# Kernel optimization log

Hardware: AMD Instinct MI355X
Metric: run time of the kernel (lower is better)

## Reference

```python
import jax, jax.numpy as jnp
import numpy as np

L, P = 8, 512
HID = 128
N_COARSE, N_FINE = 64, 128
LVIS_NEAR, LVIS_FAR = 1e-3, 0.5
S = 100.0  # 1 / fixed_s_recp


def _mlp_sdf(x, w0, b0, w1, b1, w2, b2, w3, b3):
    # x: [..., 3] -> sdf [...]
    h = jax.nn.relu(x @ w0 + b0)
    h = jax.nn.relu(h @ w1 + b1)
    h = jax.nn.relu(h @ w2 + b2)
    return (h @ w3 + b3)[..., 0]


def _sdf_to_w(sdf, s):
    # faithful to sdf_to_w: cdf -> alpha -> visibility weights via cumprod
    cdf = jax.nn.sigmoid(sdf * s)
    alpha = jnp.clip((cdf[..., :-1] - cdf[..., 1:]) / (cdf[..., :-1] + 1e-10), 0.0, None)
    ones = jnp.ones(alpha.shape[:-1] + (1,), alpha.dtype)
    shifted = jnp.concatenate([ones, 1.0 - alpha + 1e-10], axis=-1)
    return alpha * jnp.cumprod(shifted, axis=-1)[..., :-1]


def _sample_pdf(bins, weights, u):
    # standard NeRF importance sampling; bins [...,M+1], weights [...,M], u [...,N]
    weights = weights + 1e-5
    pdf = weights / jnp.sum(weights, axis=-1, keepdims=True)
    cdf = jnp.cumsum(pdf, axis=-1)
    cdf = jnp.concatenate([jnp.zeros_like(cdf[..., :1]), cdf], axis=-1)  # [...,M+1]
    # searchsorted (right) via broadcast compare: [...,N,M+1]
    inds = jnp.sum((u[..., None] >= cdf[..., None, :]).astype(jnp.int32), axis=-1)
    below = jnp.clip(inds - 1, 0, cdf.shape[-1] - 1)
    above = jnp.clip(inds, 0, cdf.shape[-1] - 1)
    cdf_b = jnp.take_along_axis(cdf, below, axis=-1)
    cdf_a = jnp.take_along_axis(cdf, above, axis=-1)
    bins_b = jnp.take_along_axis(bins, below, axis=-1)
    bins_a = jnp.take_along_axis(bins, above, axis=-1)
    denom = cdf_a - cdf_b
    denom = jnp.where(denom < 1e-5, jnp.ones_like(denom), denom)
    t = (u - cdf_b) / denom
    return bins_b + t * (bins_a - bins_b)


def setup_inputs() -> dict:
    key = jax.random.key(0)
    ks = jax.random.split(key, 8)

    def lin(k, fi, fo):
        return jax.random.normal(k, (fi, fo), jnp.float32) / jnp.sqrt(jnp.float32(fi))

    return {
        "pts": jax.random.normal(ks[0], (1, P, 3), jnp.float32) * 0.5,
        "light_posi": jax.random.normal(ks[1], (L, 3), jnp.float32) * 2.0,
        "u": jax.random.uniform(ks[2], (L, P, N_FINE), jnp.float32),
        "w0": lin(ks[3], 3, HID), "b0": jnp.zeros((HID,), jnp.float32),
        "w1": lin(ks[4], HID, HID), "b1": jnp.zeros((HID,), jnp.float32),
        "w2": lin(ks[5], HID, HID), "b2": jnp.zeros((HID,), jnp.float32),
        "w3": lin(ks[6], HID, 1), "b3": jnp.zeros((1,), jnp.float32),
    }


def reference(pts, light_posi, u, w0, b0, w1, b1, w2, b2, w3, b3):
    sdf = lambda x: _mlp_sdf(x, w0, b0, w1, b1, w2, b2, w3, b3)
    # pts: [1,P,3]; light_posi: [L,3]
    pts2l = light_posi[:, None, :] - pts  # [L,P,3]
    pts2l = pts2l / jnp.linalg.norm(pts2l, axis=-1, keepdims=True)
    t = jnp.linspace(0.0, 1.0 - 1.0 / N_COARSE, N_COARSE, dtype=jnp.float32)
    d_coarse = LVIS_NEAR * (1.0 - t) + LVIS_FAR * t  # [N_COARSE]
    d_coarse = jnp.broadcast_to(d_coarse, (pts2l.shape[0], pts.shape[1], N_COARSE))
    # coarse sample points: [L,P,Nc,3]
    pts_coarse = pts[:, :, None, :] + d_coarse[..., None] * pts2l[:, :, None, :]
    w_coarse = _sdf_to_w(sdf(pts_coarse), S)  # [L,P,Nc-1]
    d_fine = _sample_pdf(d_coarse, w_coarse, u)  # [L,P,Nf]
    d_all = jnp.sort(jnp.concatenate([d_coarse, d_fine], axis=-1), axis=-1)  # [L,P,Nc+Nf]
    pts_all = pts[:, :, None, :] + d_all[..., None] * pts2l[:, :, None, :]
    w_all = _sdf_to_w(sdf(pts_all), S)
    occu = jnp.sum(w_all, axis=-1)  # [L,P]
    return 1.0 - occu
```

## Files before the change

kernel.cpp:

```cpp
#include <hip/hip_runtime.h>
#include <math.h>

#define NL 8
#define NP 512
#define NC 64
#define NF 128
#define NALL 192
#define NRAY (NL * NP)
#define HID 128

typedef _Float16 half8 __attribute__((ext_vector_type(8)));
typedef _Float16 half4v __attribute__((ext_vector_type(4)));
typedef float floatx16 __attribute__((ext_vector_type(16)));
typedef unsigned long long ull;

#define MFMA(a, b, c) __builtin_amdgcn_mfma_f32_32x32x16_f16((a), (b), (c), 0, 0, 0)


__device__ __forceinline__ float dcoarse_at(int i) {
    float t = (float)i * 0.015625f;
    return 1e-3f * (1.0f - t) + 0.5f * t;
}

__device__ __forceinline__ floatx16 fzero16() {
    floatx16 z;
#pragma unroll
    for (int i = 0; i < 16; ++i) z[i] = 0.f;
    return z;
}
__device__ __forceinline__ half8 hzero8() {
    half8 z;
#pragma unroll
    for (int i = 0; i < 8; ++i) z[i] = (_Float16)0.f;
    return z;
}

__global__ void prep_kernel(const float* __restrict__ w1, const float* __restrict__ w2,
                            _Float16* __restrict__ Wsp) {
    int f = blockIdx.x * 256 + threadIdx.x;
    int layer = blockIdx.y;
    const float* w = layer ? w2 : w1;
    int i = f & 7, l31 = (f >> 3) & 31, lhi = (f >> 8) & 1, ks = (f >> 9) & 7, jb = f >> 12;
    int j = jb * 32 + l31;
    int k = ks * 16 + lhi * 8 + i;
    float v = w[k * 128 + j];
    _Float16 hi = (_Float16)v;
    Wsp[(layer * 2 + 0) * 16384 + f] = hi;
    Wsp[(layer * 2 + 1) * 16384 + f] = (_Float16)(v - (float)hi);
}

template<int MODE, int FASTW>
__global__ __launch_bounds__(512, 4) void mlp_kernel(
    const float* __restrict__ pts, const float* __restrict__ lights,
    const float* __restrict__ d_fine,
    const float* __restrict__ w0, const float* __restrict__ b0,
    const float* __restrict__ w1, const float* __restrict__ b1,
    const float* __restrict__ w2, const float* __restrict__ b2,
    const float* __restrict__ w3, const float* __restrict__ b3,
    const _Float16* __restrict__ Wsp,
    float* __restrict__ sdf_out)
{
    __shared__ __align__(16) _Float16 H[2 * 128 * 128];
    __shared__ _Float16 Xs[6 * 128];
    __shared__ float P2[4 * 128];

    const int tid = threadIdx.x;
    const int lane = tid & 63;
    const int wv = tid >> 6;
    const int jq = wv & 3, mh = wv >> 2;
    const int l31 = lane & 31, lhi = lane >> 5;
    const int base = blockIdx.x * 128;

    if (tid < 128) {
        int pt = base + tid;
        int ray; float d;
        if (MODE == 0) { ray = pt >> 6; d = dcoarse_at(pt & 63); }
        else           { ray = pt >> 7; d = d_fine[pt]; }
        int l = ray >> 9, p = ray & (NP - 1);
        float px = pts[p * 3 + 0], py = pts[p * 3 + 1], pz = pts[p * 3 + 2];
        float dx = lights[l * 3 + 0] - px, dy = lights[l * 3 + 1] - py, dz = lights[l * 3 + 2] - pz;
        float n = sqrtf(dx * dx + dy * dy + dz * dz);
        dx /= n; dy /= n; dz /= n;
        float xc[3] = { px + d * dx, py + d * dy, pz + d * dz };
#pragma unroll
        for (int c = 0; c < 3; ++c) {
            _Float16 h = (_Float16)xc[c];
            Xs[c * 128 + tid] = h;
            Xs[(3 + c) * 128 + tid] = (_Float16)(xc[c] - (float)h);
        }
    }

    const int m0 = mh * 64;
    const int mrow0 = m0 + l31;
    char* Hb = (char*)H;

    int rdoff[8];
#pragma unroll
    for (int ks = 0; ks < 8; ++ks) {
        int k0 = ks * 16 + lhi * 8;
        rdoff[ks] = (mrow0 * 128 + ((((k0 >> 3) ^ (mrow0 & 15)) << 3) | (k0 & 7))) * 2;
    }

    auto store_tile = [&](const floatx16& a, int mt, const float* __restrict__ bias) {
        int mrow = mrow0 + mt * 32;
#pragma unroll
        for (int g = 0; g < 4; ++g) {
            int jg = jq * 32 + 8 * g + 4 * lhi;
            half4v hq, lq;
#pragma unroll
            for (int q = 0; q < 4; ++q) {
                float v = fmaxf(a[g * 4 + q] + bias[jg + q], 0.f);
                _Float16 hi = (_Float16)v;
                hq[q] = hi;
                lq[q] = (_Float16)(v - (float)hi);
            }
            int ad = (mrow * 128 + ((((jg >> 3) ^ (mrow & 15)) << 3) | (jg & 7))) * 2;
            *(half4v*)(Hb + ad) = hq;
            *(half4v*)(Hb + ad + 32768) = lq;
        }
    };

    floatx16 acc[2];

    const int aoff = jq * 4096 + lhi * 256 + l31 * 8 + 2048;
    const _Float16* pA0h = Wsp + 0 * 16384 + aoff;
    const _Float16* pA0l = Wsp + 1 * 16384 + aoff;
    const _Float16* pA1h = Wsp + 2 * 16384 + aoff;
    const _Float16* pA1l = Wsp + 3 * 16384 + aoff;

    auto ldA_slow = [&](int L, int ks, half8& ah, half8& al) {
        const float* w = L ? w2 : w1;
        int j = jq * 32 + l31, k0 = ks * 16 + lhi * 8;
#pragma unroll
        for (int i = 0; i < 8; ++i) {
            float v = w[(k0 + i) * 128 + j];
            _Float16 hi = (_Float16)v;
            ah[i] = hi;
            al[i] = (_Float16)(v - (float)hi);
        }
    };

    half8 Ah[8], Al[8];
    auto preload4 = [&](int L, const _Float16* ph, const _Float16* pl) {
        if (FASTW) {
#pragma unroll
            for (int ks = 0; ks < 4; ++ks) {
                Ah[ks] = *(const half8*)(ph + ks * 512 - 2048);
                Al[ks] = *(const half8*)(pl + ks * 512 - 2048);
            }
        } else {
#pragma unroll
            for (int ks = 0; ks < 4; ++ks) ldA_slow(L, ks, Ah[ks], Al[ks]);
        }
    };

    auto gemm = [&](int L, const _Float16* ph, const _Float16* pl) {
        acc[0] = fzero16(); acc[1] = fzero16();
#pragma unroll
        for (int ks = 0; ks < 8; ++ks) {
            if (ks < 4) {
                if (FASTW) {
                    Ah[ks + 4] = *(const half8*)(ph + (ks + 4) * 512 - 2048);
                    Al[ks + 4] = *(const half8*)(pl + (ks + 4) * 512 - 2048);
                } else {
                    ldA_slow(L, ks + 4, Ah[ks + 4], Al[ks + 4]);
                }
            }
            char* ba = Hb + rdoff[ks];
            half8 bh0 = *(const half8*)(ba);
            half8 bh1 = *(const half8*)(ba + 8192);
            half8 bl0 = *(const half8*)(ba + 32768);
            half8 bl1 = *(const half8*)(ba + 40960);
            acc[0] = MFMA(Al[ks], bh0, acc[0]); acc[1] = MFMA(Al[ks], bh1, acc[1]);
            acc[0] = MFMA(Ah[ks], bl0, acc[0]); acc[1] = MFMA(Ah[ks], bl1, acc[1]);
            acc[0] = MFMA(Ah[ks], bh0, acc[0]); acc[1] = MFMA(Ah[ks], bh1, acc[1]);
        }
    };

    __syncthreads();

    {
        half8 a1h = hzero8(), a1l = hzero8(), bh1[2], bl1[2];
        bh1[0] = hzero8(); bh1[1] = hzero8(); bl1[0] = hzero8(); bl1[1] = hzero8();
        if (lhi == 0) {
            int j = jq * 32 + l31;
#pragma unroll
            for (int c = 0; c < 3; ++c) {
                float v = w0[c * 128 + j];
                _Float16 hi = (_Float16)v;
                a1h[c] = hi;
                a1l[c] = (_Float16)(v - (float)hi);
            }
#pragma unroll
            for (int mt = 0; mt < 2; ++mt) {
                int m = m0 + mt * 32 + l31;
#pragma unroll
                for (int c = 0; c < 3; ++c) {
                    bh1[mt][c] = Xs[c * 128 + m];
                    bl1[mt][c] = Xs[(3 + c) * 128 + m];
                }
            }
        }
        acc[0] = fzero16(); acc[1] = fzero16();
        acc[0] = MFMA(a1l, bh1[0], acc[0]); acc[1] = MFMA(a1l, bh1[1], acc[1]);
        acc[0] = MFMA(a1h, bl1[0], acc[0]); acc[1] = MFMA(a1h, bl1[1], acc[1]);
        acc[0] = MFMA(a1h, bh1[0], acc[0]); acc[1] = MFMA(a1h, bh1[1], acc[1]);
        store_tile(acc[0], 0, b0);
        store_tile(acc[1], 1, b0);
    }

    preload4(0, pA0h, pA0l);
    __syncthreads();

    gemm(0, pA0h, pA0l);
    preload4(1, pA1h, pA1l);
    __syncthreads();
    store_tile(acc[0], 0, b1);
    store_tile(acc[1], 1, b1);
    __syncthreads();

    gemm(1, pA1h, pA1l);
#pragma unroll
    for (int mt = 0; mt < 2; ++mt) {
        float p = 0.f;
#pragma unroll
        for (int g = 0; g < 4; ++g) {
            int jg = jq * 32 + 8 * g + 4 * lhi;
#pragma unroll
            for (int q = 0; q < 4; ++q) {
                float v = fmaxf(acc[mt][g * 4 + q] + b2[jg + q], 0.f);
                p = fmaf(v, w3[jg + q], p);
            }
        }
        p += __shfl_xor(p, 32);
        if (lane < 32) P2[jq * 128 + m0 + mt * 32 + l31] = p;
    }
    __syncthreads();
    if (tid < 128)
        sdf_out[base + tid] = b3[0] + P2[tid] + P2[128 + tid] + P2[256 + tid] + P2[384 + tid];
}

__global__ __launch_bounds__(256) void sample_kernel(
    const float* __restrict__ sdf_c, const float* __restrict__ u,
    float* __restrict__ d_fine, unsigned char* __restrict__ perm8) {
    const int lane = threadIdx.x & 63, wv = threadIdx.x >> 6;
    const int ray = blockIdx.x * 4 + wv;

    float sv = sdf_c[ray * NC + lane];
    float c = 1.0f / (1.0f + expf(-100.0f * sv));
    float cn = __shfl_down(c, 1);
    bool valid = lane < 63;
    float a = valid ? fmaxf((c - cn) / (c + 1e-10f), 0.f) : 0.f;
    float sh = valid ? (1.f - a + 1e-10f) : 1.f;
    float ps = sh;
#pragma unroll
    for (int off = 1; off < 64; off <<= 1) { float o = __shfl_up(ps, off); if (lane >= off) ps *= o; }
    float T = __shfl_up(ps, 1);
    if (lane == 0) T = 1.f;
    float w = valid ? (a * T + 1e-5f) : 0.f;
    float wsum = w;
#pragma unroll
    for (int off = 1; off < 64; off <<= 1) wsum += __shfl_xor(wsum, off);
    float pdf = w / wsum;
    float cs = pdf;
#pragma unroll
    for (int off = 1; off < 64; off <<= 1) { float o = __shfl_up(cs, off); if (lane >= off) cs += o; }
    float cdfv = __shfl_up(cs, 1);
    if (lane == 0) cdfv = 0.f;

    float df[2];
#pragma unroll
    for (int t = 0; t < 2; ++t) {
        float uu = u[ray * NF + t * 64 + lane];
        int lo = 0;
#pragma unroll
        for (int b = 32; b >= 1; b >>= 1) {
            float cm = __shfl(cdfv, lo + b);
            if (uu >= cm) lo += b;
        }
        int above = min(lo + 1, NC - 1);
        float cb = __shfl(cdfv, lo), ca = __shfl(cdfv, above);
        float bb = dcoarse_at(lo), ba = dcoarse_at(above);
        float denom = ca - cb;
        if (denom < 1e-5f) denom = 1.f;
        float tt = (uu - cb) / denom;
        df[t] = bb + tt * (ba - bb);
        d_fine[ray * 128 + t * 64 + lane] = df[t];
    }

    ull v[4];
    v[0] = ((ull)__float_as_uint(dcoarse_at(lane)) << 32) | (unsigned)lane;
    v[1] = ((ull)__float_as_uint(df[0]) << 32) | (unsigned)(64 + lane);
    v[2] = ((ull)__float_as_uint(df[1]) << 32) | (unsigned)(128 + lane);
    v[3] = ((ull)0x7F800000u << 32) | 255u;
    for (int k = 2; k <= 256; k <<= 1) {
        for (int j = k >> 1; j > 0; j >>= 1) {
            if (j >= 64) {
                int tj = j >> 6;
#pragma unroll
                for (int t = 0; t < 4; ++t) {
                    if ((t & tj) == 0) {
                        int t2 = t ^ tj;
                        bool asc = (((t * 64) & k) == 0);
                        ull x = v[t], y = v[t2];
                        bool sw = asc ? (x > y) : (x < y);
                        if (sw) { v[t] = y; v[t2] = x; }
                    }
                }
            } else {
#pragma unroll
                for (int t = 0; t < 4; ++t) {
                    int i = t * 64 + lane;
                    ull other = __shfl_xor(v[t], j);
                    bool lower = (lane & j) == 0;
                    bool asc = ((i & k) == 0);
                    bool takeMin = (lower == asc);
                    ull mn = v[t] < other ? v[t] : other;
                    ull mx = v[t] < other ? other : v[t];
                    v[t] = takeMin ? mn : mx;
                }
            }
        }
    }
#pragma unroll
    for (int t = 0; t < 3; ++t)
        perm8[ray * NALL + t * 64 + lane] = (unsigned char)(v[t] & 0xFFu);
}

__global__ __launch_bounds__(256) void finish_kernel(
    const float* __restrict__ sdf_c, const float* __restrict__ sdf_f,
    const unsigned char* __restrict__ perm8, float* __restrict__ out) {
    int lane = threadIdx.x & 63, wv = threadIdx.x >> 6;
    int ray = blockIdx.x * 4 + wv;
    const unsigned char* P = perm8 + (size_t)ray * NALL;
    float c[4];
#pragma unroll
    for (int t = 0; t < 4; ++t) {
        int i = lane * 3 + t;
        if (i < NALL) {
            int idx = P[i];
            float s = (idx < 64) ? sdf_c[ray * NC + idx] : sdf_f[ray * 128 + (idx - 64)];
            c[t] = 1.0f / (1.0f + expf(-100.0f * s));
        } else c[t] = 0.f;
    }
    float a[3], s[3];
#pragma unroll
    for (int t = 0; t < 3; ++t) {
        int i = lane * 3 + t;
        if (i < NALL - 1) {
            a[t] = fmaxf((c[t] - c[t + 1]) / (c[t] + 1e-10f), 0.f);
            s[t] = 1.f - a[t] + 1e-10f;
        } else { a[t] = 0.f; s[t] = 1.f; }
    }
    float chunk = s[0] * s[1] * s[2];
    float ps = chunk;
#pragma unroll
    for (int off = 1; off < 64; off <<= 1) {
        float o = __shfl_up(ps, off);
        if (lane >= off) ps *= o;
    }
    float T = __shfl_up(ps, 1);
    if (lane == 0) T = 1.f;
    float occ = a[0] * T;
    T *= s[0]; occ = fmaf(a[1], T, occ);
    T *= s[1]; occ = fmaf(a[2], T, occ);
#pragma unroll
    for (int off = 1; off < 64; off <<= 1) occ += __shfl_xor(occ, off);
    if (lane == 0) out[ray] = 1.f - occ;
}

extern "C" void kernel_launch(void* const* d_in, const int* in_sizes, int n_in,
                              void* d_out, int out_size, void* d_ws, size_t ws_size,
                              hipStream_t stream) {
    const float* pts = (const float*)d_in[0];
    const float* lights = (const float*)d_in[1];
    const float* u = (const float*)d_in[2];
    const float* w0 = (const float*)d_in[3];
    const float* b0 = (const float*)d_in[4];
    const float* w1 = (const float*)d_in[5];
    const float* b1 = (const float*)d_in[6];
    const float* w2 = (const float*)d_in[7];
    const float* b2 = (const float*)d_in[8];
    const float* w3 = (const float*)d_in[9];
    const float* b3 = (const float*)d_in[10];
    float* out = (float*)d_out;

    char* wsb = (char*)d_ws;
    float* sdf_c = (float*)wsb;
    float* sdf_f = (float*)(wsb + (size_t)NRAY * NC * 4);
    float* d_fine = (float*)(wsb + (size_t)NRAY * (NC + 128) * 4);
    unsigned char* perm8 = (unsigned char*)(wsb + (size_t)NRAY * (NC + 256) * 4);
    _Float16* Wsp = (_Float16*)(wsb + (size_t)NRAY * (NC + 256) * 4 + (size_t)NRAY * NALL);
    const size_t need = (size_t)NRAY * (NC + 256) * 4 + (size_t)NRAY * NALL
                      + (size_t)4 * 16384 * sizeof(_Float16);
    const bool fast = ws_size >= need;

    if (fast) {
        prep_kernel<<<dim3(64, 2), 256, 0, stream>>>(w1, w2, Wsp);
        mlp_kernel<0, 1><<<(NRAY * NC) / 128, 512, 0, stream>>>(
            pts, lights, nullptr, w0, b0, w1, b1, w2, b2, w3, b3, Wsp, sdf_c);
        sample_kernel<<<NRAY / 4, 256, 0, stream>>>(sdf_c, u, d_fine, perm8);
        mlp_kernel<1, 1><<<(NRAY * 128) / 128, 512, 0, stream>>>(
            pts, lights, d_fine, w0, b0, w1, b1, w2, b2, w3, b3, Wsp, sdf_f);
    } else {
        mlp_kernel<0, 0><<<(NRAY * NC) / 128, 512, 0, stream>>>(
            pts, lights, nullptr, w0, b0, w1, b1, w2, b2, w3, b3, nullptr, sdf_c);
        sample_kernel<<<NRAY / 4, 256, 0, stream>>>(sdf_c, u, d_fine, perm8);
        mlp_kernel<1, 0><<<(NRAY * 128) / 128, 512, 0, stream>>>(
            pts, lights, d_fine, w0, b0, w1, b1, w2, b2, w3, b3, nullptr, sdf_f);
    }
    finish_kernel<<<NRAY / 4, 256, 0, stream>>>(sdf_c, sdf_f, perm8, out);
}
```

Before: 243.1 us.

## Halve MLP block to 4 waves, each computing 64x64 output tile

The MLP kernel now runs 256 threads (4 waves) per 128-point block instead of 512. Each wave computes two 32-column output tiles across two 32-row tiles, so every B fragment read from LDS feeds twice as many MFMAs. This halves LDS read traffic per MFMA. The register preloading of weight A fragments is replaced by per-k-step global loads. In exchange the kernel has fewer waves per block, a larger accumulator per wave that raises register pressure, and less latency hiding on the weight loads.

Result: no change. 244.3 us (+0.5%).

```diff
diff --git a/kernel.cpp b/kernel.cpp
--- a/kernel.cpp
+++ b/kernel.cpp
@@ -50,7 +50,7 @@
 }
 
 template<int MODE, int FASTW>
-__global__ __launch_bounds__(512, 4) void mlp_kernel(
+__global__ __launch_bounds__(256, 2) void mlp_kernel(
     const float* __restrict__ pts, const float* __restrict__ lights,
     const float* __restrict__ d_fine,
     const float* __restrict__ w0, const float* __restrict__ b0,
@@ -67,7 +67,7 @@
     const int tid = threadIdx.x;
     const int lane = tid & 63;
     const int wv = tid >> 6;
-    const int jq = wv & 3, mh = wv >> 2;
+    const int jh = wv & 1, mh = wv >> 1;
     const int l31 = lane & 31, lhi = lane >> 5;
     const int base = blockIdx.x * 128;
 
@@ -101,11 +101,11 @@
         rdoff[ks] = (mrow0 * 128 + ((((k0 >> 3) ^ (mrow0 & 15)) << 3) | (k0 & 7))) * 2;
     }
 
-    auto store_tile = [&](const floatx16& a, int mt, const float* __restrict__ bias) {
+    auto store_tile = [&](const floatx16& a, int jt, int mt, const float* __restrict__ bias) {
         int mrow = mrow0 + mt * 32;
 #pragma unroll
         for (int g = 0; g < 4; ++g) {
-            int jg = jq * 32 + 8 * g + 4 * lhi;
+            int jg = jh * 64 + jt * 32 + 8 * g + 4 * lhi;
             half4v hq, lq;
 #pragma unroll
             for (int q = 0; q < 4; ++q) {
@@ -120,17 +120,22 @@
         }
     };
 
-    floatx16 acc[2];
-
-    const int aoff = jq * 4096 + lhi * 256 + l31 * 8 + 2048;
-    const _Float16* pA0h = Wsp + 0 * 16384 + aoff;
-    const _Float16* pA0l = Wsp + 1 * 16384 + aoff;
-    const _Float16* pA1h = Wsp + 2 * 16384 + aoff;
-    const _Float16* pA1l = Wsp + 3 * 16384 + aoff;
-
-    auto ldA_slow = [&](int L, int ks, half8& ah, half8& al) {
+    floatx16 acc[2][2];
+
+    const int aoff0 = (jh * 2 + 0) * 4096 + lhi * 256 + l31 * 8 + 2048;
+    const int aoff1 = (jh * 2 + 1) * 4096 + lhi * 256 + l31 * 8 + 2048;
+    const _Float16* pA0h0 = Wsp + 0 * 16384 + aoff0;
+    const _Float16* pA0l0 = Wsp + 1 * 16384 + aoff0;
+    const _Float16* pA0h1 = Wsp + 0 * 16384 + aoff1;
+    const _Float16* pA0l1 = Wsp + 1 * 16384 + aoff1;
+    const _Float16* pA1h0 = Wsp + 2 * 16384 + aoff0;
+    const _Float16* pA1l0 = Wsp + 3 * 16384 + aoff0;
+    const _Float16* pA1h1 = Wsp + 2 * 16384 + aoff1;
+    const _Float16* pA1l1 = Wsp + 3 * 16384 + aoff1;
+
+    auto ldA_slow = [&](int L, int jt, int ks, half8& ah, half8& al) {
         const float* w = L ? w2 : w1;
-        int j = jq * 32 + l31, k0 = ks * 16 + lhi * 8;
+        int j = jh * 64 + jt * 32 + l31, k0 = ks * 16 + lhi * 8;
 #pragma unroll
         for (int i = 0; i < 8; ++i) {
             float v = w[(k0 + i) * 128 + j];
@@ -140,56 +145,53 @@
         }
     };
 
-    half8 Ah[8], Al[8];
-    auto preload4 = [&](int L, const _Float16* ph, const _Float16* pl) {
-        if (FASTW) {
-#pragma unroll
-            for (int ks = 0; ks < 4; ++ks) {
-                Ah[ks] = *(const half8*)(ph + ks * 512 - 2048);
-                Al[ks] = *(const half8*)(pl + ks * 512 - 2048);
-            }
-        } else {
-#pragma unroll
-            for (int ks = 0; ks < 4; ++ks) ldA_slow(L, ks, Ah[ks], Al[ks]);
-        }
-    };
-
-    auto gemm = [&](int L, const _Float16* ph, const _Float16* pl) {
-        acc[0] = fzero16(); acc[1] = fzero16();
+    auto gemm = [&](int L, const _Float16* ph0, const _Float16* pl0,
+                    const _Float16* ph1, const _Float16* pl1) {
+        acc[0][0] = fzero16(); acc[0][1] = fzero16();
+        acc[1][0] = fzero16(); acc[1][1] = fzero16();
 #pragma unroll
         for (int ks = 0; ks < 8; ++ks) {
-            if (ks < 4) {
-                if (FASTW) {
-                    Ah[ks + 4] = *(const half8*)(ph + (ks + 4) * 512 - 2048);
-                    Al[ks + 4] = *(const half8*)(pl + (ks + 4) * 512 - 2048);
-                } else {
-                    ldA_slow(L, ks + 4, Ah[ks + 4], Al[ks + 4]);
-                }
+            half8 a0h, a0l, a1h, a1l;
+            if (FASTW) {
+                a0h = *(const half8*)(ph0 + ks * 512 - 2048);
+                a0l = *(const half8*)(pl0 + ks * 512 - 2048);
+                a1h = *(const half8*)(ph1 + ks * 512 - 2048);
+                a1l = *(const half8*)(pl1 + ks * 512 - 2048);
+            } else {
+                ldA_slow(L, 0, ks, a0h, a0l);
+                ldA_slow(L, 1, ks, a1h, a1l);
             }
             char* ba = Hb + rdoff[ks];
             half8 bh0 = *(const half8*)(ba);
             half8 bh1 = *(const half8*)(ba + 8192);
             half8 bl0 = *(const half8*)(ba + 32768);
             half8 bl1 = *(const half8*)(ba + 40960);
-            acc[0] = MFMA(Al[ks], bh0, acc[0]); acc[1] = MFMA(Al[ks], bh1, acc[1]);
-            acc[0] = MFMA(Ah[ks], bl0, acc[0]); acc[1] = MFMA(Ah[ks], bl1, acc[1]);
-            acc[0] = MFMA(Ah[ks], bh0, acc[0]); acc[1] = MFMA(Ah[ks], bh1, acc[1]);
+            acc[0][0] = MFMA(a0l, bh0, acc[0][0]); acc[0][1] = MFMA(a0l, bh1, acc[0][1]);
+            acc[1][0] = MFMA(a1l, bh0, acc[1][0]); acc[1][1] = MFMA(a1l, bh1, acc[1][1]);
+            acc[0][0] = MFMA(a0h, bl0, acc[0][0]); acc[0][1] = MFMA(a0h, bl1, acc[0][1]);
+            acc[1][0] = MFMA(a1h, bl0, acc[1][0]); acc[1][1] = MFMA(a1h, bl1, acc[1][1]);
+            acc[0][0] = MFMA(a0h, bh0, acc[0][0]); acc[0][1] = MFMA(a0h, bh1, acc[0][1]);
+            acc[1][0] = MFMA(a1h, bh0, acc[1][0]); acc[1][1] = MFMA(a1h, bh1, acc[1][1]);
         }
     };
 
     __syncthreads();
 
     {
-        half8 a1h = hzero8(), a1l = hzero8(), bh1[2], bl1[2];
+        half8 a1h[2], a1l[2], bh1[2], bl1[2];
+        a1h[0] = hzero8(); a1h[1] = hzero8(); a1l[0] = hzero8(); a1l[1] = hzero8();
         bh1[0] = hzero8(); bh1[1] = hzero8(); bl1[0] = hzero8(); bl1[1] = hzero8();
         if (lhi == 0) {
-            int j = jq * 32 + l31;
-#pragma unroll
-            for (int c = 0; c < 3; ++c) {
-                float v = w0[c * 128 + j];
-                _Float16 hi = (_Float16)v;
-                a1h[c] = hi;
-                a1l[c] = (_Float16)(v - (float)hi);
+#pragma unroll
+            for (int jt = 0; jt < 2; ++jt) {
+                int j = jh * 64 + jt * 32 + l31;
+#pragma unroll
+                for (int c = 0; c < 3; ++c) {
+                    float v = w0[c * 128 + j];
+                    _Float16 hi = (_Float16)v;
+                    a1h[jt][c] = hi;
+                    a1l[jt][c] = (_Float16)(v - (float)hi);
+                }
             }
 #pragma unroll
             for (int mt = 0; mt < 2; ++mt) {
@@ -201,39 +203,47 @@
                 }
             }
         }
-        acc[0] = fzero16(); acc[1] = fzero16();
-        acc[0] = MFMA(a1l, bh1[0], acc[0]); acc[1] = MFMA(a1l, bh1[1], acc[1]);
-        acc[0] = MFMA(a1h, bl1[0], acc[0]); acc[1] = MFMA(a1h, bl1[1], acc[1]);
-        acc[0] = MFMA(a1h, bh1[0], acc[0]); acc[1] = MFMA(a1h, bh1[1], acc[1]);
-        store_tile(acc[0], 0, b0);
-        store_tile(acc[1], 1, b0);
-    }
-
-    preload4(0, pA0h, pA0l);
+        acc[0][0] = fzero16(); acc[0][1] = fzero16();
+        acc[1][0] = fzero16(); acc[1][1] = fzero16();
+        acc[0][0] = MFMA(a1l[0], bh1[0], acc[0][0]); acc[0][1] = MFMA(a1l[0], bh1[1], acc[0][1]);
+        acc[1][0] = MFMA(a1l[1], bh1[0], acc[1][0]); acc[1][1] = MFMA(a1l[1], bh1[1], acc[1][1]);
+        acc[0][0] = MFMA(a1h[0], bl1[0], acc[0][0]); acc[0][1] = MFMA(a1h[0], bl1[1], acc[0][1]);
+        acc[1][0] = MFMA(a1h[1], bl1[0], acc[1][0]); acc[1][1] = MFMA(a1h[1], bl1[1], acc[1][1]);
+        acc[0][0] = MFMA(a1h[0], bh1[0], acc[0][0]); acc[0][1] = MFMA(a1h[0], bh1[1], acc[0][1]);
+        acc[1][0] = MFMA(a1h[1], bh1[0], acc[1][0]); acc[1][1] = MFMA(a1h[1], bh1[1], acc[1][1]);
+        store_tile(acc[0][0], 0, 0, b0);
+        store_tile(acc[0][1], 0, 1, b0);
+        store_tile(acc[1][0], 1, 0, b0);
+        store_tile(acc[1][1], 1, 1, b0);
+    }
     __syncthreads();
 
-    gemm(0, pA0h, pA0l);
-    preload4(1, pA1h, pA1l);
+    gemm(0, pA0h0, pA0l0, pA0h1, pA0l1);
     __syncthreads();
-    store_tile(acc[0], 0, b1);
-    store_tile(acc[1], 1, b1);
+    store_tile(acc[0][0], 0, 0, b1);
+    store_tile(acc[0][1], 0, 1, b1);
+    store_tile(acc[1][0], 1, 0, b1);
+    store_tile(acc[1][1], 1, 1, b1);
     __syncthreads();
 
-    gemm(1, pA1h, pA1l);
-#pragma unroll
-    for (int mt = 0; mt < 2; ++mt) {
-        float p = 0.f;
-#pragma unroll
-        for (int g = 0; g < 4; ++g) {
-            int jg = jq * 32 + 8 * g + 4 * lhi;
-#pragma unroll
-            for (int q = 0; q < 4; ++q) {
-                float v = fmaxf(acc[mt][g * 4 + q] + b2[jg + q], 0.f);
-                p = fmaf(v, w3[jg + q], p);
-            }
-        }
-        p += __shfl_xor(p, 32);
-        if (lane < 32) P2[jq * 128 + m0 + mt * 32 + l31] = p;
+    gemm(1, pA1h0, pA1l0, pA1h1, pA1l1);
+#pragma unroll
+    for (int jt = 0; jt < 2; ++jt) {
+#pragma unroll
+        for (int mt = 0; mt < 2; ++mt) {
+            float p = 0.f;
+#pragma unroll
+            for (int g = 0; g < 4; ++g) {
+                int jg = jh * 64 + jt * 32 + 8 * g + 4 * lhi;
+#pragma unroll
+                for (int q = 0; q < 4; ++q) {
+                    float v = fmaxf(acc[jt][mt][g * 4 + q] + b2[jg + q], 0.f);
+                    p = fmaf(v, w3[jg + q], p);
+                }
+            }
+            p += __shfl_xor(p, 32);
+            if (lane < 32) P2[(jh * 2 + jt) * 128 + m0 + mt * 32 + l31] = p;
+        }
     }
     __syncthreads();
     if (tid < 128)
@@ -397,16 +407,16 @@
 
     if (fast) {
         prep_kernel<<<dim3(64, 2), 256, 0, stream>>>(w1, w2, Wsp);
-        mlp_kernel<0, 1><<<(NRAY * NC) / 128, 512, 0, stream>>>(
+        mlp_kernel<0, 1><<<(NRAY * NC) / 128, 256, 0, stream>>>(
             pts, lights, nullptr, w0, b0, w1, b1, w2, b2, w3, b3, Wsp, sdf_c);
         sample_kernel<<<NRAY / 4, 256, 0, stream>>>(sdf_c, u, d_fine, perm8);
-        mlp_kernel<1, 1><<<(NRAY * 128) / 128, 512, 0, stream>>>(
+        mlp_kernel<1, 1><<<(NRAY * 128) / 128, 256, 0, stream>>>(
             pts, lights, d_fine, w0, b0, w1, b1, w2, b2, w3, b3, Wsp, sdf_f);
     } else {
-        mlp_kernel<0, 0><<<(NRAY * NC) / 128, 512, 0, stream>>>(
+        mlp_kernel<0, 0><<<(NRAY * NC) / 128, 256, 0, stream>>>(
             pts, lights, nullptr, w0, b0, w1, b1, w2, b2, w3, b3, nullptr, sdf_c);
         sample_kernel<<<NRAY / 4, 256, 0, stream>>>(sdf_c, u, d_fine, perm8);
-        mlp_kernel<1, 0><<<(NRAY * 128) / 128, 512, 0, stream>>>(
+        mlp_kernel<1, 0><<<(NRAY * 128) / 128, 256, 0, stream>>>(
             pts, lights, d_fine, w0, b0, w1, b1, w2, b2, w3, b3, nullptr, sdf_f);
     }
     finish_kernel<<<NRAY / 4, 256, 0, stream>>>(sdf_c, sdf_f, perm8, out);
```

## Fuse importance sampling and final compositing into the MLP kernels

Applied to the files above, without the earlier changes.

The sampling step (CDF, inverse-CDF search, bitonic sort into a permutation) now runs as a tail of the coarse MLP kernel, and the final visibility compositing runs as a tail of the fine MLP kernel, using the fine SDF values still held in shared memory. This removes two kernel launches and the global round trip for the fine SDF buffer. The A-weight register preload across GEMMs is also dropped in favour of per-step loads, which cuts register pressure but exposes load latency. Only a few waves do the tail work while the rest of each 512-thread block sits idle.

Result: slower. 262.8 us (+8.1%).

```diff
diff --git a/kernel.cpp b/kernel.cpp
--- a/kernel.cpp
+++ b/kernel.cpp
@@ -52,13 +52,14 @@
 template<int MODE, int FASTW>
 __global__ __launch_bounds__(512, 4) void mlp_kernel(
     const float* __restrict__ pts, const float* __restrict__ lights,
-    const float* __restrict__ d_fine,
     const float* __restrict__ w0, const float* __restrict__ b0,
     const float* __restrict__ w1, const float* __restrict__ b1,
     const float* __restrict__ w2, const float* __restrict__ b2,
     const float* __restrict__ w3, const float* __restrict__ b3,
     const _Float16* __restrict__ Wsp,
-    float* __restrict__ sdf_out)
+    float* __restrict__ sdf_c, float* __restrict__ d_fine,
+    const float* __restrict__ u, unsigned char* __restrict__ perm8,
+    float* __restrict__ out)
 {
     __shared__ __align__(16) _Float16 H[2 * 128 * 128];
     __shared__ _Float16 Xs[6 * 128];
@@ -140,40 +141,25 @@
         }
     };
 
-    half8 Ah[8], Al[8];
-    auto preload4 = [&](int L, const _Float16* ph, const _Float16* pl) {
-        if (FASTW) {
-#pragma unroll
-            for (int ks = 0; ks < 4; ++ks) {
-                Ah[ks] = *(const half8*)(ph + ks * 512 - 2048);
-                Al[ks] = *(const half8*)(pl + ks * 512 - 2048);
-            }
-        } else {
-#pragma unroll
-            for (int ks = 0; ks < 4; ++ks) ldA_slow(L, ks, Ah[ks], Al[ks]);
-        }
-    };
-
     auto gemm = [&](int L, const _Float16* ph, const _Float16* pl) {
         acc[0] = fzero16(); acc[1] = fzero16();
 #pragma unroll
         for (int ks = 0; ks < 8; ++ks) {
-            if (ks < 4) {
-                if (FASTW) {
-                    Ah[ks + 4] = *(const half8*)(ph + (ks + 4) * 512 - 2048);
-                    Al[ks + 4] = *(const half8*)(pl + (ks + 4) * 512 - 2048);
-                } else {
-                    ldA_slow(L, ks + 4, Ah[ks + 4], Al[ks + 4]);
-                }
+            half8 ah, al;
+            if (FASTW) {
+                ah = *(const half8*)(ph + ks * 512 - 2048);
+                al = *(const half8*)(pl + ks * 512 - 2048);
+            } else {
+                ldA_slow(L, ks, ah, al);
             }
             char* ba = Hb + rdoff[ks];
             half8 bh0 = *(const half8*)(ba);
             half8 bh1 = *(const half8*)(ba + 8192);
             half8 bl0 = *(const half8*)(ba + 32768);
             half8 bl1 = *(const half8*)(ba + 40960);
-            acc[0] = MFMA(Al[ks], bh0, acc[0]); acc[1] = MFMA(Al[ks], bh1, acc[1]);
-            acc[0] = MFMA(Ah[ks], bl0, acc[0]); acc[1] = MFMA(Ah[ks], bl1, acc[1]);
-            acc[0] = MFMA(Ah[ks], bh0, acc[0]); acc[1] = MFMA(Ah[ks], bh1, acc[1]);
+            acc[0] = MFMA(al, bh0, acc[0]); acc[1] = MFMA(al, bh1, acc[1]);
+            acc[0] = MFMA(ah, bl0, acc[0]); acc[1] = MFMA(ah, bl1, acc[1]);
+            acc[0] = MFMA(ah, bh0, acc[0]); acc[1] = MFMA(ah, bh1, acc[1]);
         }
     };
 
@@ -208,12 +194,9 @@
         store_tile(acc[0], 0, b0);
         store_tile(acc[1], 1, b0);
     }
-
-    preload4(0, pA0h, pA0l);
     __syncthreads();
 
     gemm(0, pA0h, pA0l);
-    preload4(1, pA1h, pA1l);
     __syncthreads();
     store_tile(acc[0], 0, b1);
     store_tile(acc[1], 1, b1);
@@ -236,137 +219,136 @@
         if (lane < 32) P2[jq * 128 + m0 + mt * 32 + l31] = p;
     }
     __syncthreads();
-    if (tid < 128)
-        sdf_out[base + tid] = b3[0] + P2[tid] + P2[128 + tid] + P2[256 + tid] + P2[384 + tid];
-}
-
-__global__ __launch_bounds__(256) void sample_kernel(
-    const float* __restrict__ sdf_c, const float* __restrict__ u,
-    float* __restrict__ d_fine, unsigned char* __restrict__ perm8) {
-    const int lane = threadIdx.x & 63, wv = threadIdx.x >> 6;
-    const int ray = blockIdx.x * 4 + wv;
-
-    float sv = sdf_c[ray * NC + lane];
-    float c = 1.0f / (1.0f + expf(-100.0f * sv));
-    float cn = __shfl_down(c, 1);
-    bool valid = lane < 63;
-    float a = valid ? fmaxf((c - cn) / (c + 1e-10f), 0.f) : 0.f;
-    float sh = valid ? (1.f - a + 1e-10f) : 1.f;
-    float ps = sh;
-#pragma unroll
-    for (int off = 1; off < 64; off <<= 1) { float o = __shfl_up(ps, off); if (lane >= off) ps *= o; }
-    float T = __shfl_up(ps, 1);
-    if (lane == 0) T = 1.f;
-    float w = valid ? (a * T + 1e-5f) : 0.f;
-    float wsum = w;
-#pragma unroll
-    for (int off = 1; off < 64; off <<= 1) wsum += __shfl_xor(wsum, off);
-    float pdf = w / wsum;
-    float cs = pdf;
-#pragma unroll
-    for (int off = 1; off < 64; off <<= 1) { float o = __shfl_up(cs, off); if (lane >= off) cs += o; }
-    float cdfv = __shfl_up(cs, 1);
-    if (lane == 0) cdfv = 0.f;
-
-    float df[2];
-#pragma unroll
-    for (int t = 0; t < 2; ++t) {
-        float uu = u[ray * NF + t * 64 + lane];
-        int lo = 0;
-#pragma unroll
-        for (int b = 32; b >= 1; b >>= 1) {
-            float cm = __shfl(cdfv, lo + b);
-            if (uu >= cm) lo += b;
-        }
-        int above = min(lo + 1, NC - 1);
-        float cb = __shfl(cdfv, lo), ca = __shfl(cdfv, above);
-        float bb = dcoarse_at(lo), ba = dcoarse_at(above);
-        float denom = ca - cb;
-        if (denom < 1e-5f) denom = 1.f;
-        float tt = (uu - cb) / denom;
-        df[t] = bb + tt * (ba - bb);
-        d_fine[ray * 128 + t * 64 + lane] = df[t];
-    }
-
-    ull v[4];
-    v[0] = ((ull)__float_as_uint(dcoarse_at(lane)) << 32) | (unsigned)lane;
-    v[1] = ((ull)__float_as_uint(df[0]) << 32) | (unsigned)(64 + lane);
-    v[2] = ((ull)__float_as_uint(df[1]) << 32) | (unsigned)(128 + lane);
-    v[3] = ((ull)0x7F800000u << 32) | 255u;
-    for (int k = 2; k <= 256; k <<= 1) {
-        for (int j = k >> 1; j > 0; j >>= 1) {
-            if (j >= 64) {
-                int tj = j >> 6;
-#pragma unroll
-                for (int t = 0; t < 4; ++t) {
-                    if ((t & tj) == 0) {
-                        int t2 = t ^ tj;
-                        bool asc = (((t * 64) & k) == 0);
-                        ull x = v[t], y = v[t2];
-                        bool sw = asc ? (x > y) : (x < y);
-                        if (sw) { v[t] = y; v[t2] = x; }
+    if (tid < 128) {
+        float s = b3[0] + P2[tid] + P2[128 + tid] + P2[256 + tid] + P2[384 + tid];
+        if (MODE == 0) sdf_c[base + tid] = s;
+        P2[tid] = s;
+    }
+    __syncthreads();
+
+    if (MODE == 0) {
+        if (wv < 2) {
+            const int ray = blockIdx.x * 2 + wv;
+            float sv = P2[wv * 64 + lane];
+            float c = 1.0f / (1.0f + expf(-100.0f * sv));
+            float cn = __shfl_down(c, 1);
+            bool valid = lane < 63;
+            float a = valid ? fmaxf((c - cn) / (c + 1e-10f), 0.f) : 0.f;
+            float sh = valid ? (1.f - a + 1e-10f) : 1.f;
+            float ps = sh;
+#pragma unroll
+            for (int off = 1; off < 64; off <<= 1) { float o = __shfl_up(ps, off); if (lane >= off) ps *= o; }
+            float T = __shfl_up(ps, 1);
+            if (lane == 0) T = 1.f;
+            float w = valid ? (a * T + 1e-5f) : 0.f;
+            float wsum = w;
+#pragma unroll
+            for (int off = 1; off < 64; off <<= 1) wsum += __shfl_xor(wsum, off);
+            float pdf = w / wsum;
+            float cs = pdf;
+#pragma unroll
+            for (int off = 1; off < 64; off <<= 1) { float o = __shfl_up(cs, off); if (lane >= off) cs += o; }
+            float cdfv = __shfl_up(cs, 1);
+            if (lane == 0) cdfv = 0.f;
+
+            float df[2];
+#pragma unroll
+            for (int t = 0; t < 2; ++t) {
+                float uu = u[ray * NF + t * 64 + lane];
+                int lo = 0;
+#pragma unroll
+                for (int b = 32; b >= 1; b >>= 1) {
+                    float cm = __shfl(cdfv, lo + b);
+                    if (uu >= cm) lo += b;
+                }
+                int above = min(lo + 1, NC - 1);
+                float cb = __shfl(cdfv, lo), ca = __shfl(cdfv, above);
+                float bb = dcoarse_at(lo), ba = dcoarse_at(above);
+                float denom = ca - cb;
+                if (denom < 1e-5f) denom = 1.f;
+                float tt = (uu - cb) / denom;
+                df[t] = bb + tt * (ba - bb);
+                d_fine[ray * 128 + t * 64 + lane] = df[t];
+            }
+
+            ull v[4];
+            v[0] = ((ull)__float_as_uint(dcoarse_at(lane)) << 32) | (unsigned)lane;
+            v[1] = ((ull)__float_as_uint(df[0]) << 32) | (unsigned)(64 + lane);
+            v[2] = ((ull)__float_as_uint(df[1]) << 32) | (unsigned)(128 + lane);
+            v[3] = ((ull)0x7F800000u << 32) | 255u;
+            for (int k = 2; k <= 256; k <<= 1) {
+                for (int j = k >> 1; j > 0; j >>= 1) {
+                    if (j >= 64) {
+                        int tj = j >> 6;
+#pragma unroll
+                        for (int t = 0; t < 4; ++t) {
+                            if ((t & tj) == 0) {
+                                int t2 = t ^ tj;
+                                bool asc = (((t * 64) & k) == 0);
+                                ull x = v[t], y = v[t2];
+                                bool sw = asc ? (x > y) : (x < y);
+                                if (sw) { v[t] = y; v[t2] = x; }
+                            }
+                        }
+                    } else {
+#pragma unroll
+                        for (int t = 0; t < 4; ++t) {
+                            int i = t * 64 + lane;
+                            ull other = __shfl_xor(v[t], j);
+                            bool lower = (lane & j) == 0;
+                            bool asc = ((i & k) == 0);
+                            bool takeMin = (lower == asc);
+                            ull mn = v[t] < other ? v[t] : other;
+                            ull mx = v[t] < other ? other : v[t];
+                            v[t] = takeMin ? mn : mx;
+                        }
                     }
                 }
-            } else {
-#pragma unroll
-                for (int t = 0; t < 4; ++t) {
-                    int i = t * 64 + lane;
-                    ull other = __shfl_xor(v[t], j);
-                    bool lower = (lane & j) == 0;
-                    bool asc = ((i & k) == 0);
-                    bool takeMin = (lower == asc);
-                    ull mn = v[t] < other ? v[t] : other;
-                    ull mx = v[t] < other ? other : v[t];
-                    v[t] = takeMin ? mn : mx;
-                }
-            }
-        }
-    }
-#pragma unroll
-    for (int t = 0; t < 3; ++t)
-        perm8[ray * NALL + t * 64 + lane] = (unsigned char)(v[t] & 0xFFu);
-}
-
-__global__ __launch_bounds__(256) void finish_kernel(
-    const float* __restrict__ sdf_c, const float* __restrict__ sdf_f,
-    const unsigned char* __restrict__ perm8, float* __restrict__ out) {
-    int lane = threadIdx.x & 63, wv = threadIdx.x >> 6;
-    int ray = blockIdx.x * 4 + wv;
-    const unsigned char* P = perm8 + (size_t)ray * NALL;
-    float c[4];
-#pragma unroll
-    for (int t = 0; t < 4; ++t) {
-        int i = lane * 3 + t;
-        if (i < NALL) {
-            int idx = P[i];
-            float s = (idx < 64) ? sdf_c[ray * NC + idx] : sdf_f[ray * 128 + (idx - 64)];
-            c[t] = 1.0f / (1.0f + expf(-100.0f * s));
-        } else c[t] = 0.f;
-    }
-    float a[3], s[3];
-#pragma unroll
-    for (int t = 0; t < 3; ++t) {
-        int i = lane * 3 + t;
-        if (i < NALL - 1) {
-            a[t] = fmaxf((c[t] - c[t + 1]) / (c[t] + 1e-10f), 0.f);
-            s[t] = 1.f - a[t] + 1e-10f;
-        } else { a[t] = 0.f; s[t] = 1.f; }
-    }
-    float chunk = s[0] * s[1] * s[2];
-    float ps = chunk;
-#pragma unroll
-    for (int off = 1; off < 64; off <<= 1) {
-        float o = __shfl_up(ps, off);
-        if (lane >= off) ps *= o;
-    }
-    float T = __shfl_up(ps, 1);
-    if (lane == 0) T = 1.f;
-    float occ = a[0] * T;
-    T *= s[0]; occ = fmaf(a[1], T, occ);
-    T *= s[1]; occ = fmaf(a[2], T, occ);
-#pragma unroll
-    for (int off = 1; off < 64; off <<= 1) occ += __shfl_xor(occ, off);
-    if (lane == 0) out[ray] = 1.f - occ;
+            }
+#pragma unroll
+            for (int t = 0; t < 3; ++t)
+                perm8[ray * NALL + t * 64 + lane] = (unsigned char)(v[t] & 0xFFu);
+        }
+    } else {
+        if (wv == 0) {
+            const int ray = blockIdx.x;
+            const unsigned char* P = perm8 + (size_t)ray * NALL;
+            float c[4];
+#pragma unroll
+            for (int t = 0; t < 4; ++t) {
+                int i = lane * 3 + t;
+                if (i < NALL) {
+                    int idx = P[i];
+                    float s = (idx < 64) ? sdf_c[ray * NC + idx] : P2[idx - 64];
+                    c[t] = 1.0f / (1.0f + expf(-100.0f * s));
+                } else c[t] = 0.f;
+            }
+            float a[3], sv3[3];
+#pragma unroll
+            for (int t = 0; t < 3; ++t) {
+                int i = lane * 3 + t;
+                if (i < NALL - 1) {
+                    a[t] = fmaxf((c[t] - c[t + 1]) / (c[t] + 1e-10f), 0.f);
+                    sv3[t] = 1.f - a[t] + 1e-10f;
+                } else { a[t] = 0.f; sv3[t] = 1.f; }
+            }
+            float chunk = sv3[0] * sv3[1] * sv3[2];
+            float ps = chunk;
+#pragma unroll
+            for (int off = 1; off < 64; off <<= 1) {
+                float o = __shfl_up(ps, off);
+                if (lane >= off) ps *= o;
+            }
+            float T = __shfl_up(ps, 1);
+            if (lane == 0) T = 1.f;
+            float occ = a[0] * T;
+            T *= sv3[0]; occ = fmaf(a[1], T, occ);
+            T *= sv3[1]; occ = fmaf(a[2], T, occ);
+#pragma unroll
+            for (int off = 1; off < 64; off <<= 1) occ += __shfl_xor(occ, off);
+            if (lane == 0) out[ray] = 1.f - occ;
+        }
+    }
 }
 
 extern "C" void kernel_launch(void* const* d_in, const int* in_sizes, int n_in,
@@ -387,7 +369,6 @@
 
     char* wsb = (char*)d_ws;
     float* sdf_c = (float*)wsb;
-    float* sdf_f = (float*)(wsb + (size_t)NRAY * NC * 4);
     float* d_fine = (float*)(wsb + (size_t)NRAY * (NC + 128) * 4);
     unsigned char* perm8 = (unsigned char*)(wsb + (size_t)NRAY * (NC + 256) * 4);
     _Float16* Wsp = (_Float16*)(wsb + (size_t)NRAY * (NC + 256) * 4 + (size_t)NRAY * NALL);
@@ -398,16 +379,17 @@
     if (fast) {
         prep_kernel<<<dim3(64, 2), 256, 0, stream>>>(w1, w2, Wsp);
         mlp_kernel<0, 1><<<(NRAY * NC) / 128, 512, 0, stream>>>(
-            pts, lights, nullptr, w0, b0, w1, b1, w2, b2, w3, b3, Wsp, sdf_c);
-        sample_kernel<<<NRAY / 4, 256, 0, stream>>>(sdf_c, u, d_fine, perm8);
-        mlp_kernel<1, 1><<<(NRAY * 128) / 128, 512, 0, stream>>>(
-            pts, lights, d_fine, w0, b0, w1, b1, w2, b2, w3, b3, Wsp, sdf_f);
+            pts, lights, w0, b0, w1, b1, w2, b2, w3, b3, Wsp,
+            sdf_c, d_fine, u, perm8, out);
+        mlp_kernel<1, 1><<<NRAY, 512, 0, stream>>>(
+            pts, lights, w0, b0, w1, b1, w2, b2, w3, b3, Wsp,
+            sdf_c, d_fine, u, perm8, out);
     } else {
         mlp_kernel<0, 0><<<(NRAY * NC) / 128, 512, 0, stream>>>(
-            pts, lights, nullptr, w0, b0, w1, b1, w2, b2, w3, b3, nullptr, sdf_c);
-        sample_kernel<<<NRAY / 4, 256, 0, stream>>>(sdf_c, u, d_fine, perm8);
-        mlp_kernel<1, 0><<<(NRAY * 128) / 128, 512, 0, stream>>>(
-            pts, lights, d_fine, w0, b0, w1, b1, w2, b2, w3, b3, nullptr, sdf_f);
-    }
-    finish_kernel<<<NRAY / 4, 256, 0, stream>>>(sdf_c, sdf_f, perm8, out);
-}
+            pts, lights, w0, b0, w1, b1, w2, b2, w3, b3, nullptr,
+            sdf_c, d_fine, u, perm8, out);
+        mlp_kernel<1, 0><<<NRAY, 512, 0, stream>>>(
+            pts, lights, w0, b0, w1, b1, w2, b2, w3, b3, nullptr,
+            sdf_c, d_fine, u, perm8, out);
+    }
+}
```
